# Performance work log

Measured on AMD Instinct MI355X. Metric: run time of the kernel, lower is better.

The kernel has to match this reference:

```python
import jax, jax.numpy as jnp
import numpy as np

B, T, D, H, L = 64, 4096, 128, 128, 2


def setup_inputs() -> dict:
    key = jax.random.key(0)
    ks = jax.random.split(key, 9)
    s = 1.0 / np.sqrt(H)
    return {
        "x": jax.random.normal(ks[0], (B, T, D), dtype=jnp.float32),
        "W_ih0": jax.random.normal(ks[1], (3 * H, D), dtype=jnp.float32) * s,
        "W_hh0": jax.random.normal(ks[2], (3 * H, H), dtype=jnp.float32) * s,
        "b_ih0": jax.random.normal(ks[3], (3 * H,), dtype=jnp.float32) * s,
        "b_hh0": jax.random.normal(ks[4], (3 * H,), dtype=jnp.float32) * s,
        "W_ih1": jax.random.normal(ks[5], (3 * H, H), dtype=jnp.float32) * s,
        "W_hh1": jax.random.normal(ks[6], (3 * H, H), dtype=jnp.float32) * s,
        "b_ih1": jax.random.normal(ks[7], (3 * H,), dtype=jnp.float32) * s,
        "b_hh1": jax.random.normal(ks[8], (3 * H,), dtype=jnp.float32) * s,
    }


def _gru_cell(h, xt, W_ih, W_hh, b_ih, b_hh):
    # torch.nn.GRUCell math; gates packed as [r, z, n] along 3H.
    gi = xt @ W_ih.T + b_ih            # [B, 3H]
    gh = h @ W_hh.T + b_hh             # [B, 3H]
    i_r, i_z, i_n = jnp.split(gi, 3, axis=-1)
    h_r, h_z, h_n = jnp.split(gh, 3, axis=-1)
    r = jax.nn.sigmoid(i_r + h_r)
    z = jax.nn.sigmoid(i_z + h_z)
    n = jnp.tanh(i_n + r * h_n)
    return (1.0 - z) * n + z * h


def reference(x, W_ih0, W_hh0, b_ih0, b_hh0, W_ih1, W_hh1, b_ih1, b_hh1):
    h0 = jnp.zeros((L, x.shape[0], H), dtype=x.dtype)
    params = ((W_ih0, W_hh0, b_ih0, b_hh0), (W_ih1, W_hh1, b_ih1, b_hh1))

    def step(h, xt):
        # h: [L, B, H]; xt: [B, D]
        inp = xt
        new_h = []
        for l in range(L):
            hl = _gru_cell(h[l], inp, *params[l])
            new_h.append(hl)
            inp = hl
        return jnp.stack(new_h, axis=0), None

    xs = jnp.swapaxes(x, 0, 1)  # [T, B, D]
    h_final, _ = jax.lax.scan(step, h0, xs)
    return h_final  # [L, B, H]
```

## Files before the change

kernel.cpp:

```cpp
#include <hip/hip_runtime.h>


#define Tlen 4096
#define Hd   128
#define Bsz  64

typedef __attribute__((ext_vector_type(8))) short short8;
typedef __attribute__((ext_vector_type(4))) short short4v;
typedef __attribute__((ext_vector_type(4))) float float4v;
typedef __attribute__((ext_vector_type(2))) unsigned int uint2v;

#define MFMA16(a, b, c) __builtin_amdgcn_mfma_f32_16x16x32_bf16((a), (b), (c), 0, 0, 0)

static __device__ __forceinline__ float fast_exp2(float x) {
#if __has_builtin(__builtin_amdgcn_exp2f)
  return __builtin_amdgcn_exp2f(x);
#else
  return exp2f(x);
#endif
}
static __device__ __forceinline__ float fast_rcp(float x) {
  return __builtin_amdgcn_rcpf(x);
}
static __device__ __forceinline__ short f2bf(float f) {
  unsigned u = __builtin_bit_cast(unsigned, f);
  u = (u + 0x7FFFu + ((u >> 16) & 1u)) >> 16;
  return (short)u;
}
static __device__ __forceinline__ unsigned pk2bf(float a, float b) {
#if __has_builtin(__builtin_amdgcn_cvt_pk_bf16_f32)
  auto v = __builtin_amdgcn_cvt_pk_bf16_f32(a, b);
  return __builtin_bit_cast(unsigned, v);
#else
  return (unsigned)(unsigned short)f2bf(a) | ((unsigned)(unsigned short)f2bf(b) << 16);
#endif
}
static __device__ __forceinline__ short8 loadw8(const float* __restrict__ p) {
  short8 r;
  #pragma unroll
  for (int j = 0; j < 8; ++j) r[j] = f2bf(p[j]);
  return r;
}

#define XB   0
#define H0B  4096
#define H1B  8192
#define BLK  2048

__global__ __launch_bounds__(512, 2) void gru_scan(
    const float* __restrict__ x,
    const float* __restrict__ Wih0, const float* __restrict__ Whh0,
    const float* __restrict__ bih0, const float* __restrict__ bhh0,
    const float* __restrict__ Wih1, const float* __restrict__ Whh1,
    const float* __restrict__ bih1, const float* __restrict__ bhh1,
    float* __restrict__ out) {
  __shared__ alignas(16) short Abuf[12288];

  const int tid   = threadIdx.x;
  const int wave  = tid >> 6;
  const int lane  = tid & 63;
  const int lc    = lane & 15;
  const int quad  = lane >> 4;
  const int q8    = quad * 8;
  const int lane8 = lane * 8;
  const int bbase = blockIdx.x * 16;

  const int wgrp = wave >> 2;
  const int w4   = wave & 3;

  const float* Wi = wgrp ? Wih1 : Wih0;
  const float* Wh = wgrp ? Whh1 : Whh0;
  const float* bi = wgrp ? bih1 : bih0;
  const float* bh = wgrp ? bhh1 : bhh0;

  short8 fxr[2][4], fxz[2][4], fxn[2][4];
  short8 fhr[2][4], fhz[2][4], fhn[2][4];
  float kr[2], kz[2], ki[2], kh[2];
  const float nL  = -1.44269504088896f;
  const float n2L = -2.88539008177793f;
  #pragma unroll
  for (int G = 0; G < 2; ++G) {
    const int c = 32 * w4 + 16 * G + lc;
    #pragma unroll
    for (int s = 0; s < 4; ++s) {
      const int k = 32 * s + q8;
      fxr[G][s] = loadw8(Wi + (c)       * Hd + k);
      fxz[G][s] = loadw8(Wi + (128 + c) * Hd + k);
      fxn[G][s] = loadw8(Wi + (256 + c) * Hd + k);
      fhr[G][s] = loadw8(Wh + (c)       * Hd + k);
      fhz[G][s] = loadw8(Wh + (128 + c) * Hd + k);
      fhn[G][s] = loadw8(Wh + (256 + c) * Hd + k);
    }
    kr[G] = nL  * (bi[c] + bh[c]);
    kz[G] = nL  * (bi[128 + c] + bh[128 + c]);
    ki[G] = n2L * bi[256 + c];
    kh[G] = n2L * bh[256 + c];
  }

  const int hsel = wgrp ? H1B : H0B;
  const int isel = wgrp ? H0B : XB;

  int hw[2];
  #pragma unroll
  for (int G = 0; G < 2; ++G)
    hw[G] = w4 * 512 + (2 * G + (lc >> 3)) * 128 + (lc & 7);

  const int xrow = tid >> 5;
  const int xk0  = 4 * (tid & 31);
  const int xwoff = (xk0 >> 5) * 512 + ((xk0 >> 3) & 3) * 128 + xrow * 8 + (xk0 & 7);
  const float* xg = x + (size_t)(bbase + xrow) * (Tlen * Hd) + xk0;

  const int glo = wgrp ? 2 : 0;
  const int ghi = glo + Tlen;

  {
    int* zb = (int*)Abuf;
    #pragma unroll
    for (int i = 0; i < 8; ++i) zb[2048 + tid + 512 * i] = 0;
    const float4v v0 = *(const float4v*)(xg);
    const float4v v1 = *(const float4v*)(xg + Hd);
    uint2v p0 = {pk2bf(v0[0], v0[1]), pk2bf(v0[2], v0[3])};
    uint2v p1 = {pk2bf(v1[0], v1[1]), pk2bf(v1[2], v1[3])};
    *(short4v*)&Abuf[XB + xwoff]       = __builtin_bit_cast(short4v, p0);
    *(short4v*)&Abuf[XB + BLK + xwoff] = __builtin_bit_cast(short4v, p1);
  }
  __syncthreads();

  const float4v Z4 = {0.f, 0.f, 0.f, 0.f};
  float4v ar[2], az[2], an[2], ah[2];
  float4v hp[2] = {Z4, Z4};

  #pragma unroll
  for (int G = 0; G < 2; ++G) { ar[G] = Z4; az[G] = Z4; an[G] = Z4; ah[G] = Z4; }
  #pragma unroll
  for (int s = 0; s < 4; ++s) {
    const short8 a = *(const short8*)&Abuf[isel + s * 512 + lane8];
    #pragma unroll
    for (int G = 0; G < 2; ++G) {
      ar[G] = MFMA16(a, fxr[G][s], ar[G]);
      az[G] = MFMA16(a, fxz[G][s], az[G]);
      an[G] = MFMA16(a, fxn[G][s], an[G]);
    }
  }

  for (int t = 0; t < Tlen + 2; ++t) {
    const int par  = (t & 1) * BLK;
    const int parx = BLK - par;

    const int tn = (t + 2 < Tlen) ? (t + 2) : (Tlen - 1);
    const float4v xv = *(const float4v*)(xg + (size_t)tn * Hd);
    const int hrd = hsel + parx;
    #pragma unroll
    for (int s = 0; s < 4; ++s) {
      const short8 a = *(const short8*)&Abuf[hrd + s * 512 + lane8];
      #pragma unroll
      for (int G = 0; G < 2; ++G) {
        ar[G] = MFMA16(a, fhr[G][s], ar[G]);
        az[G] = MFMA16(a, fhz[G][s], az[G]);
        ah[G] = MFMA16(a, fhn[G][s], ah[G]);
      }
    }
    __syncthreads();

    if (t >= glo && t < ghi) {
      const int wr = hsel + par;
      #pragma unroll
      for (int G = 0; G < 2; ++G) {
        #pragma unroll
        for (int i = 0; i < 4; ++i) {
          const float er = fast_exp2(fmaf(ar[G][i], nL, kr[G]));
          const float rr = fast_rcp(1.0f + er);
          const float ez = fast_exp2(fmaf(az[G][i], nL, kz[G]));
          const float zz = fast_rcp(1.0f + ez);
          float vv = fmaf(rr, fmaf(ah[G][i], n2L, kh[G]),
                          fmaf(an[G][i], n2L, ki[G]));
          vv = fminf(vv, 126.0f);
          const float e2 = fast_exp2(vv);
          const float nn = (1.0f - e2) * fast_rcp(1.0f + e2);
          const float hn = fmaf(zz, hp[G][i] - nn, nn);
          hp[G][i] = hn;
          Abuf[wr + hw[G] + (quad * 4 + i) * 8] = f2bf(hn);
        }
      }
    }
    {
      uint2v pp = {pk2bf(xv[0], xv[1]), pk2bf(xv[2], xv[3])};
      *(short4v*)&Abuf[XB + par + xwoff] = __builtin_bit_cast(short4v, pp);
    }
    const int ird = isel + parx;
    #pragma unroll
    for (int G = 0; G < 2; ++G) { ar[G] = Z4; az[G] = Z4; an[G] = Z4; ah[G] = Z4; }
    #pragma unroll
    for (int s = 0; s < 4; ++s) {
      const short8 a = *(const short8*)&Abuf[ird + s * 512 + lane8];
      #pragma unroll
      for (int G = 0; G < 2; ++G) {
        ar[G] = MFMA16(a, fxr[G][s], ar[G]);
        az[G] = MFMA16(a, fxz[G][s], az[G]);
        an[G] = MFMA16(a, fxn[G][s], an[G]);
      }
    }
    __syncthreads();
  }

  #pragma unroll
  for (int G = 0; G < 2; ++G) {
    const int u = 32 * w4 + 16 * G + lc;
    #pragma unroll
    for (int i = 0; i < 4; ++i) {
      const int b = bbase + quad * 4 + i;
      out[wgrp * (Bsz * Hd) + b * Hd + u] = hp[G][i];
    }
  }
}

extern "C" void kernel_launch(void* const* d_in, const int* in_sizes, int n_in,
                              void* d_out, int out_size, void* d_ws, size_t ws_size,
                              hipStream_t stream) {
  (void)in_sizes; (void)n_in; (void)out_size; (void)d_ws; (void)ws_size;
  gru_scan<<<4, 512, 0, stream>>>(
      (const float*)d_in[0],
      (const float*)d_in[1], (const float*)d_in[2],
      (const float*)d_in[3], (const float*)d_in[4],
      (const float*)d_in[5], (const float*)d_in[6],
      (const float*)d_in[7], (const float*)d_in[8],
      (float*)d_out);
}
```

Measured before the change: 7.178 ms.

## Merge per-step input and hidden GEMMs into one phase with a single barrier

The time loop is restructured so each step loads both input and hidden operands, does all MFMAs, then the gate math, with one __syncthreads per step instead of two. Layer 1 now runs one step behind layer 0 instead of two. The MFMA operands are swapped so weights are the A operand, which transposes the output layout. This lets each lane write four consecutive hidden units with one packed bf16 store instead of four scalar stores. The cost is a longer serial chain between barriers, with input and hidden MFMAs no longer overlapped across the barrier, plus a partial unroll by 2.

Result: slower. 15.48 ms (+115.7%).

```diff
diff --git a/kernel.cpp b/kernel.cpp
--- a/kernel.cpp
+++ b/kernel.cpp
@@ -73,143 +73,138 @@
   const float* bi = wgrp ? bih1 : bih0;
   const float* bh = wgrp ? bhh1 : bhh0;
 
-  short8 fxr[2][4], fxz[2][4], fxn[2][4];
-  short8 fhr[2][4], fhz[2][4], fhn[2][4];
-  float kr[2], kz[2], ki[2], kh[2];
+  short8 wxr[2][4], wxz[2][4], wxn[2][4];
+  short8 whr[2][4], whz[2][4], whn[2][4];
+  float kr[2][4], kz[2][4], ki[2][4], kh[2][4];
   const float nL  = -1.44269504088896f;
   const float n2L = -2.88539008177793f;
   #pragma unroll
-  for (int G = 0; G < 2; ++G) {
-    const int c = 32 * w4 + 16 * G + lc;
+  for (int T = 0; T < 2; ++T) {
+    const int U0 = 32 * w4 + 16 * T;
     #pragma unroll
     for (int s = 0; s < 4; ++s) {
       const int k = 32 * s + q8;
-      fxr[G][s] = loadw8(Wi + (c)       * Hd + k);
-      fxz[G][s] = loadw8(Wi + (128 + c) * Hd + k);
-      fxn[G][s] = loadw8(Wi + (256 + c) * Hd + k);
-      fhr[G][s] = loadw8(Wh + (c)       * Hd + k);
-      fhz[G][s] = loadw8(Wh + (128 + c) * Hd + k);
-      fhn[G][s] = loadw8(Wh + (256 + c) * Hd + k);
-    }
-    kr[G] = nL  * (bi[c] + bh[c]);
-    kz[G] = nL  * (bi[128 + c] + bh[128 + c]);
-    ki[G] = n2L * bi[256 + c];
-    kh[G] = n2L * bh[256 + c];
-  }
-
-  const int hsel = wgrp ? H1B : H0B;
-  const int isel = wgrp ? H0B : XB;
-
-  int hw[2];
-  #pragma unroll
-  for (int G = 0; G < 2; ++G)
-    hw[G] = w4 * 512 + (2 * G + (lc >> 3)) * 128 + (lc & 7);
-
-  const int xrow = tid >> 5;
-  const int xk0  = 4 * (tid & 31);
+      wxr[T][s] = loadw8(Wi + (U0 + lc) * Hd + k);
+      wxz[T][s] = loadw8(Wi + (128 + U0 + lc) * Hd + k);
+      wxn[T][s] = loadw8(Wi + (256 + U0 + lc) * Hd + k);
+      whr[T][s] = loadw8(Wh + (U0 + lc) * Hd + k);
+      whz[T][s] = loadw8(Wh + (128 + U0 + lc) * Hd + k);
+      whn[T][s] = loadw8(Wh + (256 + U0 + lc) * Hd + k);
+    }
+    #pragma unroll
+    for (int i = 0; i < 4; ++i) {
+      const int U = U0 + quad * 4 + i;
+      kr[T][i] = nL  * (bi[U] + bh[U]);
+      kz[T][i] = nL  * (bi[128 + U] + bh[128 + U]);
+      ki[T][i] = n2L * bi[256 + U];
+      kh[T][i] = n2L * bh[256 + U];
+    }
+  }
+
+  const int ib0 = wgrp ? H0B : XB;
+  const int hb0 = wgrp ? H1B : H0B;
+
+  int wroff[2];
+  #pragma unroll
+  for (int T = 0; T < 2; ++T)
+    wroff[T] = w4 * 512 + (2 * T + (quad >> 1)) * 128 + lc * 8 + 4 * (quad & 1);
+
+  const int xrow  = tid >> 5;
+  const int xk0   = 4 * (tid & 31);
   const int xwoff = (xk0 >> 5) * 512 + ((xk0 >> 3) & 3) * 128 + xrow * 8 + (xk0 & 7);
   const float* xg = x + (size_t)(bbase + xrow) * (Tlen * Hd) + xk0;
 
-  const int glo = wgrp ? 2 : 0;
-  const int ghi = glo + Tlen;
-
   {
     int* zb = (int*)Abuf;
     #pragma unroll
     for (int i = 0; i < 8; ++i) zb[2048 + tid + 512 * i] = 0;
     const float4v v0 = *(const float4v*)(xg);
-    const float4v v1 = *(const float4v*)(xg + Hd);
-    uint2v p0 = {pk2bf(v0[0], v0[1]), pk2bf(v0[2], v0[3])};
-    uint2v p1 = {pk2bf(v1[0], v1[1]), pk2bf(v1[2], v1[3])};
-    *(short4v*)&Abuf[XB + xwoff]       = __builtin_bit_cast(short4v, p0);
-    *(short4v*)&Abuf[XB + BLK + xwoff] = __builtin_bit_cast(short4v, p1);
+    uint2v pp = {pk2bf(v0[0], v0[1]), pk2bf(v0[2], v0[3])};
+    *(short4v*)&Abuf[XB + xwoff] = __builtin_bit_cast(short4v, pp);
   }
   __syncthreads();
 
   const float4v Z4 = {0.f, 0.f, 0.f, 0.f};
-  float4v ar[2], az[2], an[2], ah[2];
   float4v hp[2] = {Z4, Z4};
 
-  #pragma unroll
-  for (int G = 0; G < 2; ++G) { ar[G] = Z4; az[G] = Z4; an[G] = Z4; ah[G] = Z4; }
-  #pragma unroll
-  for (int s = 0; s < 4; ++s) {
-    const short8 a = *(const short8*)&Abuf[isel + s * 512 + lane8];
-    #pragma unroll
-    for (int G = 0; G < 2; ++G) {
-      ar[G] = MFMA16(a, fxr[G][s], ar[G]);
-      az[G] = MFMA16(a, fxz[G][s], az[G]);
-      an[G] = MFMA16(a, fxn[G][s], an[G]);
-    }
-  }
-
-  for (int t = 0; t < Tlen + 2; ++t) {
-    const int par  = (t & 1) * BLK;
-    const int parx = BLK - par;
-
-    const int tn = (t + 2 < Tlen) ? (t + 2) : (Tlen - 1);
+  #pragma unroll 2
+  for (int t = 0; t <= Tlen; ++t) {
+    const int ibase = ib0 + ((t + wgrp) & 1) * BLK;
+    const int hbase = hb0 + ((t + 1 + wgrp) & 1) * BLK;
+    const int wbase = hb0 + ((t + wgrp) & 1) * BLK;
+
+    const int tn = (t + 1 < Tlen) ? (t + 1) : (Tlen - 1);
     const float4v xv = *(const float4v*)(xg + (size_t)tn * Hd);
-    const int hrd = hsel + parx;
-    #pragma unroll
-    for (int s = 0; s < 4; ++s) {
-      const short8 a = *(const short8*)&Abuf[hrd + s * 512 + lane8];
+
+    short8 bfi[4], bfh[4];
+    #pragma unroll
+    for (int s = 0; s < 4; ++s)
+      bfi[s] = *(const short8*)&Abuf[ibase + s * 512 + lane8];
+    #pragma unroll
+    for (int s = 0; s < 4; ++s)
+      bfh[s] = *(const short8*)&Abuf[hbase + s * 512 + lane8];
+
+    float4v aR[2], aZ[2], aIN[2], aHN[2];
+    #pragma unroll
+    for (int T = 0; T < 2; ++T) {
+      aR[T]  = MFMA16(wxr[T][0], bfi[0], Z4);
+      aZ[T]  = MFMA16(wxz[T][0], bfi[0], Z4);
+      aIN[T] = MFMA16(wxn[T][0], bfi[0], Z4);
+      aHN[T] = MFMA16(whn[T][0], bfh[0], Z4);
       #pragma unroll
-      for (int G = 0; G < 2; ++G) {
-        ar[G] = MFMA16(a, fhr[G][s], ar[G]);
-        az[G] = MFMA16(a, fhz[G][s], az[G]);
-        ah[G] = MFMA16(a, fhn[G][s], ah[G]);
-      }
-    }
-    __syncthreads();
-
-    if (t >= glo && t < ghi) {
-      const int wr = hsel + par;
+      for (int s = 1; s < 4; ++s) {
+        aR[T]  = MFMA16(wxr[T][s], bfi[s], aR[T]);
+        aZ[T]  = MFMA16(wxz[T][s], bfi[s], aZ[T]);
+        aIN[T] = MFMA16(wxn[T][s], bfi[s], aIN[T]);
+        aHN[T] = MFMA16(whn[T][s], bfh[s], aHN[T]);
+      }
       #pragma unroll
-      for (int G = 0; G < 2; ++G) {
+      for (int s = 0; s < 4; ++s) {
+        aR[T] = MFMA16(whr[T][s], bfh[s], aR[T]);
+        aZ[T] = MFMA16(whz[T][s], bfh[s], aZ[T]);
+      }
+    }
+
+    const bool gv = wgrp ? (t >= 1) : (t < Tlen);
+    #pragma unroll
+    for (int T = 0; T < 2; ++T) {
+      float hn[4];
+      #pragma unroll
+      for (int i = 0; i < 4; ++i) {
+        const float er = fast_exp2(fmaf(aR[T][i], nL, kr[T][i]));
+        const float rr = fast_rcp(1.0f + er);
+        const float ez = fast_exp2(fmaf(aZ[T][i], nL, kz[T][i]));
+        const float zz = fast_rcp(1.0f + ez);
+        float vv = fmaf(rr, fmaf(aHN[T][i], n2L, kh[T][i]),
+                        fmaf(aIN[T][i], n2L, ki[T][i]));
+        vv = fminf(vv, 126.0f);
+        const float e2 = fast_exp2(vv);
+        const float nn = (1.0f - e2) * fast_rcp(1.0f + e2);
+        hn[i] = fmaf(zz, hp[T][i] - nn, nn);
+      }
+      if (gv) {
         #pragma unroll
-        for (int i = 0; i < 4; ++i) {
-          const float er = fast_exp2(fmaf(ar[G][i], nL, kr[G]));
-          const float rr = fast_rcp(1.0f + er);
-          const float ez = fast_exp2(fmaf(az[G][i], nL, kz[G]));
-          const float zz = fast_rcp(1.0f + ez);
-          float vv = fmaf(rr, fmaf(ah[G][i], n2L, kh[G]),
-                          fmaf(an[G][i], n2L, ki[G]));
-          vv = fminf(vv, 126.0f);
-          const float e2 = fast_exp2(vv);
-          const float nn = (1.0f - e2) * fast_rcp(1.0f + e2);
-          const float hn = fmaf(zz, hp[G][i] - nn, nn);
-          hp[G][i] = hn;
-          Abuf[wr + hw[G] + (quad * 4 + i) * 8] = f2bf(hn);
-        }
-      }
-    }
+        for (int i = 0; i < 4; ++i) hp[T][i] = hn[i];
+        uint2v pp = {pk2bf(hn[0], hn[1]), pk2bf(hn[2], hn[3])};
+        *(short4v*)&Abuf[wbase + wroff[T]] = __builtin_bit_cast(short4v, pp);
+      }
+    }
+
     {
       uint2v pp = {pk2bf(xv[0], xv[1]), pk2bf(xv[2], xv[3])};
-      *(short4v*)&Abuf[XB + par + xwoff] = __builtin_bit_cast(short4v, pp);
-    }
-    const int ird = isel + parx;
-    #pragma unroll
-    for (int G = 0; G < 2; ++G) { ar[G] = Z4; az[G] = Z4; an[G] = Z4; ah[G] = Z4; }
-    #pragma unroll
-    for (int s = 0; s < 4; ++s) {
-      const short8 a = *(const short8*)&Abuf[ird + s * 512 + lane8];
-      #pragma unroll
-      for (int G = 0; G < 2; ++G) {
-        ar[G] = MFMA16(a, fxr[G][s], ar[G]);
-        az[G] = MFMA16(a, fxz[G][s], az[G]);
-        an[G] = MFMA16(a, fxn[G][s], an[G]);
-      }
+      *(short4v*)&Abuf[XB + ((t + 1) & 1) * BLK + xwoff] =
+          __builtin_bit_cast(short4v, pp);
     }
     __syncthreads();
   }
 
   #pragma unroll
-  for (int G = 0; G < 2; ++G) {
-    const int u = 32 * w4 + 16 * G + lc;
+  for (int T = 0; T < 2; ++T) {
     #pragma unroll
     for (int i = 0; i < 4; ++i) {
-      const int b = bbase + quad * 4 + i;
-      out[wgrp * (Bsz * Hd) + b * Hd + u] = hp[G][i];
+      const int u = 32 * w4 + 16 * T + quad * 4 + i;
+      const int b = bbase + lc;
+      out[wgrp * (Bsz * Hd) + b * Hd + u] = hp[T][i];
     }
   }
 }
```

## Precompute layer-0 input projection in a parallel pre-kernel and restructure scan

Applied to the files above, without the earlier changes.

Adds a separate highly parallel kernel that computes x@W_ih0 for all timesteps into workspace as bf16, taking that GEMM off the sequential recurrence. The scan kernel now has all 8 waves handle both layers for a 16-unit slice each, with layer-1 hidden-dependent work overlapped with layer 0. It prefetches the precomputed gates two steps ahead and falls back to the old kernel when workspace is too small. This adds global traffic for the gate buffer and extra bf16 rounding of the input gates.

Measured after the change: 7.391 ms. +3.0%, slower.

```diff
diff --git a/kernel.cpp b/kernel.cpp
--- a/kernel.cpp
+++ b/kernel.cpp
@@ -9,6 +9,7 @@
 typedef __attribute__((ext_vector_type(4))) short short4v;
 typedef __attribute__((ext_vector_type(4))) float float4v;
 typedef __attribute__((ext_vector_type(2))) unsigned int uint2v;
+typedef __attribute__((ext_vector_type(4))) unsigned int uint4v;
 
 #define MFMA16(a, b, c) __builtin_amdgcn_mfma_f32_16x16x32_bf16((a), (b), (c), 0, 0, 0)
 
@@ -41,13 +42,252 @@
   for (int j = 0; j < 8; ++j) r[j] = f2bf(p[j]);
   return r;
 }
-
-#define XB   0
-#define H0B  4096
-#define H1B  8192
+static __device__ __forceinline__ float bfsel(uint2v d, int i) {
+  const unsigned u = (i & 1) ? (d[i >> 1] & 0xFFFF0000u) : (d[i >> 1] << 16);
+  return __builtin_bit_cast(float, u);
+}
+
+__global__ __launch_bounds__(512, 2) void gru_pre(
+    const float* __restrict__ x, const float* __restrict__ Wih0,
+    short* __restrict__ G) {
+  const int tid  = threadIdx.x;
+  const int w    = tid >> 6;
+  const int lane = tid & 63;
+  const int lc   = lane & 15;
+  const int quad = lane >> 4;
+  const int q8   = quad * 8;
+  const int bb   = blockIdx.x & 3;
+  const int c    = blockIdx.x >> 2;
+
+  short8 fr[4], fz[4], fn[4];
+  #pragma unroll
+  for (int s = 0; s < 4; ++s) {
+    const int k = 32 * s + q8;
+    fr[s] = loadw8(Wih0 + (16 * w + lc) * Hd + k);
+    fz[s] = loadw8(Wih0 + (128 + 16 * w + lc) * Hd + k);
+    fn[s] = loadw8(Wih0 + (256 + 16 * w + lc) * Hd + k);
+  }
+  const float* xrow = x + (size_t)(bb * 16 + lc) * (Tlen * Hd);
+  const float4v Z4 = {0.f, 0.f, 0.f, 0.f};
+
+  for (int tt = 0; tt < 128; ++tt) {
+    const int t = c * 128 + tt;
+    short8 bx[4];
+    #pragma unroll
+    for (int s = 0; s < 4; ++s) {
+      const float* p = xrow + (size_t)t * Hd + 32 * s + q8;
+      const float4v lo = *(const float4v*)p;
+      const float4v hi = *(const float4v*)(p + 4);
+      uint4v u = {pk2bf(lo[0], lo[1]), pk2bf(lo[2], lo[3]),
+                  pk2bf(hi[0], hi[1]), pk2bf(hi[2], hi[3])};
+      bx[s] = __builtin_bit_cast(short8, u);
+    }
+    float4v gr = Z4, gz = Z4, gn = Z4;
+    #pragma unroll
+    for (int s = 0; s < 4; ++s) {
+      gr = MFMA16(fr[s], bx[s], gr);
+      gz = MFMA16(fz[s], bx[s], gz);
+      gn = MFMA16(fn[s], bx[s], gn);
+    }
+    const size_t base = ((((size_t)bb * Tlen + t) * 8 + w) * 3) * 256;
+    uint2v pr = {pk2bf(gr[0], gr[1]), pk2bf(gr[2], gr[3])};
+    uint2v pz = {pk2bf(gz[0], gz[1]), pk2bf(gz[2], gz[3])};
+    uint2v pn = {pk2bf(gn[0], gn[1]), pk2bf(gn[2], gn[3])};
+    *(uint2v*)&G[base + 0 * 256 + lane * 4] = pr;
+    *(uint2v*)&G[base + 1 * 256 + lane * 4] = pz;
+    *(uint2v*)&G[base + 2 * 256 + lane * 4] = pn;
+  }
+}
+
+#define CH0  0
+#define CH1  4096
 #define BLK  2048
 
 __global__ __launch_bounds__(512, 2) void gru_scan(
+    const float* __restrict__ Whh0,
+    const float* __restrict__ bih0, const float* __restrict__ bhh0,
+    const float* __restrict__ Wih1, const float* __restrict__ Whh1,
+    const float* __restrict__ bih1, const float* __restrict__ bhh1,
+    const short* __restrict__ G, float* __restrict__ out) {
+  __shared__ alignas(16) short Abuf[8192];
+
+  const int tid   = threadIdx.x;
+  const int w     = tid >> 6;
+  const int lane  = tid & 63;
+  const int lc    = lane & 15;
+  const int quad  = lane >> 4;
+  const int q8    = quad * 8;
+  const int lane8 = lane * 8;
+  const int bbase = blockIdx.x * 16;
+
+  short8 whr0[4], whz0[4], whn0[4];
+  short8 wxr1[4], wxz1[4], wxn1[4];
+  short8 whr1[4], whz1[4], whn1[4];
+  #pragma unroll
+  for (int s = 0; s < 4; ++s) {
+    const int k = 32 * s + q8;
+    const int ur = 16 * w + lc, uz = 128 + 16 * w + lc, un = 256 + 16 * w + lc;
+    whr0[s] = loadw8(Whh0 + ur * Hd + k);
+    whz0[s] = loadw8(Whh0 + uz * Hd + k);
+    whn0[s] = loadw8(Whh0 + un * Hd + k);
+    wxr1[s] = loadw8(Wih1 + ur * Hd + k);
+    wxz1[s] = loadw8(Wih1 + uz * Hd + k);
+    wxn1[s] = loadw8(Wih1 + un * Hd + k);
+    whr1[s] = loadw8(Whh1 + ur * Hd + k);
+    whz1[s] = loadw8(Whh1 + uz * Hd + k);
+    whn1[s] = loadw8(Whh1 + un * Hd + k);
+  }
+
+  const float nL  = -1.44269504088896f;
+  const float n2L = -2.88539008177793f;
+  float kr0[4], kz0[4], ki0[4], kh0[4], kr1[4], kz1[4], ki1[4], kh1[4];
+  #pragma unroll
+  for (int i = 0; i < 4; ++i) {
+    const int u = 16 * w + quad * 4 + i;
+    kr0[i] = nL  * (bih0[u] + bhh0[u]);
+    kz0[i] = nL  * (bih0[128 + u] + bhh0[128 + u]);
+    ki0[i] = n2L * bih0[256 + u];
+    kh0[i] = n2L * bhh0[256 + u];
+    kr1[i] = nL  * (bih1[u] + bhh1[u]);
+    kz1[i] = nL  * (bih1[128 + u] + bhh1[128 + u]);
+    ki1[i] = n2L * bih1[256 + u];
+    kh1[i] = n2L * bhh1[256 + u];
+  }
+
+  const int wroff = (w >> 1) * 512 + ((2 * w + (quad >> 1)) & 3) * 128 +
+                    lc * 8 + 4 * (quad & 1);
+
+  const char* Gp = (const char*)G;
+  const size_t gbase = (((size_t)blockIdx.x * Tlen * 8 + w) * 3) * 512 + lane * 8;
+
+  {
+    int* zb = (int*)Abuf;
+    #pragma unroll
+    for (int i = 0; i < 8; ++i) zb[tid + 512 * i] = 0;
+  }
+  uint2v G2[2][3];
+  #pragma unroll
+  for (int g = 0; g < 3; ++g) {
+    G2[0][g] = *(const uint2v*)(Gp + gbase + g * 512);
+    G2[1][g] = *(const uint2v*)(Gp + gbase + 12288 + g * 512);
+  }
+  __syncthreads();
+
+  const float4v Z4 = {0.f, 0.f, 0.f, 0.f};
+  float4v aR = Z4, aZ = Z4, aHN = Z4;
+  float4v cR = Z4, cZ = Z4, cIN = Z4, cHN = Z4;
+  float h0p[4] = {0.f, 0.f, 0.f, 0.f};
+  float h1p[4] = {0.f, 0.f, 0.f, 0.f};
+
+  #pragma unroll 2
+  for (int t = 0; t < Tlen + 2; ++t) {
+    const int p = t & 1;
+
+    short8 hf[4];
+    #pragma unroll
+    for (int s = 0; s < 4; ++s)
+      hf[s] = *(const short8*)&Abuf[CH0 + (p ^ 1) * BLK + s * 512 + lane8];
+
+    if (t >= 2) {
+      float hn[4];
+      #pragma unroll
+      for (int i = 0; i < 4; ++i) {
+        const float er = fast_exp2(fmaf(cR[i], nL, kr1[i]));
+        const float rr = fast_rcp(1.0f + er);
+        const float ez = fast_exp2(fmaf(cZ[i], nL, kz1[i]));
+        const float zz = fast_rcp(1.0f + ez);
+        float vv = fmaf(rr, fmaf(cHN[i], n2L, kh1[i]),
+                        fmaf(cIN[i], n2L, ki1[i]));
+        vv = fminf(vv, 126.0f);
+        const float e2 = fast_exp2(vv);
+        const float nn = (1.0f - e2) * fast_rcp(1.0f + e2);
+        hn[i] = fmaf(zz, h1p[i] - nn, nn);
+        h1p[i] = hn[i];
+      }
+      uint2v pp = {pk2bf(hn[0], hn[1]), pk2bf(hn[2], hn[3])};
+      *(short4v*)&Abuf[CH1 + p * BLK + wroff] = __builtin_bit_cast(short4v, pp);
+    }
+
+    aR  = MFMA16(whr0[0], hf[0], Z4);
+    aZ  = MFMA16(whz0[0], hf[0], Z4);
+    aHN = MFMA16(whn0[0], hf[0], Z4);
+    cR  = MFMA16(wxr1[0], hf[0], Z4);
+    cZ  = MFMA16(wxz1[0], hf[0], Z4);
+    cIN = MFMA16(wxn1[0], hf[0], Z4);
+    #pragma unroll
+    for (int s = 1; s < 4; ++s) {
+      aR  = MFMA16(whr0[s], hf[s], aR);
+      aZ  = MFMA16(whz0[s], hf[s], aZ);
+      aHN = MFMA16(whn0[s], hf[s], aHN);
+      cR  = MFMA16(wxr1[s], hf[s], cR);
+      cZ  = MFMA16(wxz1[s], hf[s], cZ);
+      cIN = MFMA16(wxn1[s], hf[s], cIN);
+    }
+    __syncthreads();
+
+    short8 gf[4];
+    #pragma unroll
+    for (int s = 0; s < 4; ++s)
+      gf[s] = *(const short8*)&Abuf[CH1 + p * BLK + s * 512 + lane8];
+
+    if (t < Tlen) {
+      float hn[4];
+      #pragma unroll
+      for (int i = 0; i < 4; ++i) {
+        const float gr = bfsel(G2[p][0], i);
+        const float gz = bfsel(G2[p][1], i);
+        const float gn = bfsel(G2[p][2], i);
+        const float er = fast_exp2(fmaf(aR[i] + gr, nL, kr0[i]));
+        const float rr = fast_rcp(1.0f + er);
+        const float ez = fast_exp2(fmaf(aZ[i] + gz, nL, kz0[i]));
+        const float zz = fast_rcp(1.0f + ez);
+        float vv = fmaf(rr, fmaf(aHN[i], n2L, kh0[i]),
+                        fmaf(gn, n2L, ki0[i]));
+        vv = fminf(vv, 126.0f);
+        const float e2 = fast_exp2(vv);
+        const float nn = (1.0f - e2) * fast_rcp(1.0f + e2);
+        hn[i] = fmaf(zz, h0p[i] - nn, nn);
+        h0p[i] = hn[i];
+      }
+      uint2v pp = {pk2bf(hn[0], hn[1]), pk2bf(hn[2], hn[3])};
+      *(short4v*)&Abuf[CH0 + p * BLK + wroff] = __builtin_bit_cast(short4v, pp);
+    }
+
+    cHN = MFMA16(whn1[0], gf[0], Z4);
+    cR  = MFMA16(whr1[0], gf[0], cR);
+    cZ  = MFMA16(whz1[0], gf[0], cZ);
+    #pragma unroll
+    for (int s = 1; s < 4; ++s) {
+      cHN = MFMA16(whn1[s], gf[s], cHN);
+      cR  = MFMA16(whr1[s], gf[s], cR);
+      cZ  = MFMA16(whz1[s], gf[s], cZ);
+    }
+
+    {
+      const int tg = (t + 2 < Tlen) ? (t + 2) : (Tlen - 1);
+      const size_t go = gbase + (size_t)tg * 12288;
+      #pragma unroll
+      for (int g = 0; g < 3; ++g)
+        G2[p][g] = *(const uint2v*)(Gp + go + g * 512);
+    }
+    __syncthreads();
+  }
+
+  #pragma unroll
+  for (int i = 0; i < 4; ++i) {
+    const int u = 16 * w + quad * 4 + i;
+    const int b = bbase + lc;
+    out[b * Hd + u]            = h0p[i];
+    out[Bsz * Hd + b * Hd + u] = h1p[i];
+  }
+}
+
+#define FXB   0
+#define FH0B  4096
+#define FH1B  8192
+#define FBLK  2048
+
+__global__ __launch_bounds__(512, 2) void gru_scan_fb(
     const float* __restrict__ x,
     const float* __restrict__ Wih0, const float* __restrict__ Whh0,
     const float* __restrict__ bih0, const float* __restrict__ bhh0,
@@ -64,7 +304,6 @@
   const int q8    = quad * 8;
   const int lane8 = lane * 8;
   const int bbase = blockIdx.x * 16;
-
   const int wgrp = wave >> 2;
   const int w4   = wave & 3;
 
@@ -79,40 +318,35 @@
   const float nL  = -1.44269504088896f;
   const float n2L = -2.88539008177793f;
   #pragma unroll
-  for (int G = 0; G < 2; ++G) {
-    const int c = 32 * w4 + 16 * G + lc;
+  for (int Gg = 0; Gg < 2; ++Gg) {
+    const int c = 32 * w4 + 16 * Gg + lc;
     #pragma unroll
     for (int s = 0; s < 4; ++s) {
       const int k = 32 * s + q8;
-      fxr[G][s] = loadw8(Wi + (c)       * Hd + k);
-      fxz[G][s] = loadw8(Wi + (128 + c) * Hd + k);
-      fxn[G][s] = loadw8(Wi + (256 + c) * Hd + k);
-      fhr[G][s] = loadw8(Wh + (c)       * Hd + k);
-      fhz[G][s] = loadw8(Wh + (128 + c) * Hd + k);
-      fhn[G][s] = loadw8(Wh + (256 + c) * Hd + k);
-    }
-    kr[G] = nL  * (bi[c] + bh[c]);
-    kz[G] = nL  * (bi[128 + c] + bh[128 + c]);
-    ki[G] = n2L * bi[256 + c];
-    kh[G] = n2L * bh[256 + c];
-  }
-
-  const int hsel = wgrp ? H1B : H0B;
-  const int isel = wgrp ? H0B : XB;
-
+      fxr[Gg][s] = loadw8(Wi + (c) * Hd + k);
+      fxz[Gg][s] = loadw8(Wi + (128 + c) * Hd + k);
+      fxn[Gg][s] = loadw8(Wi + (256 + c) * Hd + k);
+      fhr[Gg][s] = loadw8(Wh + (c) * Hd + k);
+      fhz[Gg][s] = loadw8(Wh + (128 + c) * Hd + k);
+      fhn[Gg][s] = loadw8(Wh + (256 + c) * Hd + k);
+    }
+    kr[Gg] = nL  * (bi[c] + bh[c]);
+    kz[Gg] = nL  * (bi[128 + c] + bh[128 + c]);
+    ki[Gg] = n2L * bi[256 + c];
+    kh[Gg] = n2L * bh[256 + c];
+  }
+  const int hsel = wgrp ? FH1B : FH0B;
+  const int isel = wgrp ? FH0B : FXB;
   int hw[2];
   #pragma unroll
-  for (int G = 0; G < 2; ++G)
-    hw[G] = w4 * 512 + (2 * G + (lc >> 3)) * 128 + (lc & 7);
-
+  for (int Gg = 0; Gg < 2; ++Gg)
+    hw[Gg] = w4 * 512 + (2 * Gg + (lc >> 3)) * 128 + (lc & 7);
   const int xrow = tid >> 5;
   const int xk0  = 4 * (tid & 31);
   const int xwoff = (xk0 >> 5) * 512 + ((xk0 >> 3) & 3) * 128 + xrow * 8 + (xk0 & 7);
   const float* xg = x + (size_t)(bbase + xrow) * (Tlen * Hd) + xk0;
-
   const int glo = wgrp ? 2 : 0;
   const int ghi = glo + Tlen;
-
   {
     int* zb = (int*)Abuf;
     #pragma unroll
@@ -121,32 +355,28 @@
     const float4v v1 = *(const float4v*)(xg + Hd);
     uint2v p0 = {pk2bf(v0[0], v0[1]), pk2bf(v0[2], v0[3])};
     uint2v p1 = {pk2bf(v1[0], v1[1]), pk2bf(v1[2], v1[3])};
-    *(short4v*)&Abuf[XB + xwoff]       = __builtin_bit_cast(short4v, p0);
-    *(short4v*)&Abuf[XB + BLK + xwoff] = __builtin_bit_cast(short4v, p1);
+    *(short4v*)&Abuf[FXB + xwoff]        = __builtin_bit_cast(short4v, p0);
+    *(short4v*)&Abuf[FXB + FBLK + xwoff] = __builtin_bit_cast(short4v, p1);
   }
   __syncthreads();
-
   const float4v Z4 = {0.f, 0.f, 0.f, 0.f};
   float4v ar[2], az[2], an[2], ah[2];
   float4v hp[2] = {Z4, Z4};
-
-  #pragma unroll
-  for (int G = 0; G < 2; ++G) { ar[G] = Z4; az[G] = Z4; an[G] = Z4; ah[G] = Z4; }
+  #pragma unroll
+  for (int Gg = 0; Gg < 2; ++Gg) { ar[Gg] = Z4; az[Gg] = Z4; an[Gg] = Z4; ah[Gg] = Z4; }
   #pragma unroll
   for (int s = 0; s < 4; ++s) {
     const short8 a = *(const short8*)&Abuf[isel + s * 512 + lane8];
     #pragma unroll
-    for (int G = 0; G < 2; ++G) {
-      ar[G] = MFMA16(a, fxr[G][s], ar[G]);
-      az[G] = MFMA16(a, fxz[G][s], az[G]);
-      an[G] = MFMA16(a, fxn[G][s], an[G]);
-    }
-  }
-
+    for (int Gg = 0; Gg < 2; ++Gg) {
+      ar[Gg] = MFMA16(a, fxr[Gg][s], ar[Gg]);
+      az[Gg] = MFMA16(a, fxz[Gg][s], az[Gg]);
+      an[Gg] = MFMA16(a, fxn[Gg][s], an[Gg]);
+    }
+  }
   for (int t = 0; t < Tlen + 2; ++t) {
-    const int par  = (t & 1) * BLK;
-    const int parx = BLK - par;
-
+    const int par  = (t & 1) * FBLK;
+    const int parx = FBLK - par;
     const int tn = (t + 2 < Tlen) ? (t + 2) : (Tlen - 1);
     const float4v xv = *(const float4v*)(xg + (size_t)tn * Hd);
     const int hrd = hsel + parx;
@@ -154,62 +384,60 @@
     for (int s = 0; s < 4; ++s) {
       const short8 a = *(const short8*)&Abuf[hrd + s * 512 + lane8];
       #pragma unroll
-      for (int G = 0; G < 2; ++G) {
-        ar[G] = MFMA16(a, fhr[G][s], ar[G]);
-        az[G] = MFMA16(a, fhz[G][s], az[G]);
-        ah[G] = MFMA16(a, fhn[G][s], ah[G]);
+      for (int Gg = 0; Gg < 2; ++Gg) {
+        ar[Gg] = MFMA16(a, fhr[Gg][s], ar[Gg]);
+        az[Gg] = MFMA16(a, fhz[Gg][s], az[Gg]);
+        ah[Gg] = MFMA16(a, fhn[Gg][s], ah[Gg]);
       }
     }
     __syncthreads();
-
     if (t >= glo && t < ghi) {
       const int wr = hsel + par;
       #pragma unroll
-      for (int G = 0; G < 2; ++G) {
+      for (int Gg = 0; Gg < 2; ++Gg) {
         #pragma unroll
         for (int i = 0; i < 4; ++i) {
-          const float er = fast_exp2(fmaf(ar[G][i], nL, kr[G]));
+          const float er = fast_exp2(fmaf(ar[Gg][i], nL, kr[Gg]));
           const float rr = fast_rcp(1.0f + er);
-          const float ez = fast_exp2(fmaf(az[G][i], nL, kz[G]));
+          const float ez = fast_exp2(fmaf(az[Gg][i], nL, kz[Gg]));
           const float zz = fast_rcp(1.0f + ez);
-          float vv = fmaf(rr, fmaf(ah[G][i], n2L, kh[G]),
-                          fmaf(an[G][i], n2L, ki[G]));
+          float vv = fmaf(rr, fmaf(ah[Gg][i], n2L, kh[Gg]),
+                          fmaf(an[Gg][i], n2L, ki[Gg]));
           vv = fminf(vv, 126.0f);
           const float e2 = fast_exp2(vv);
           const float nn = (1.0f - e2) * fast_rcp(1.0f + e2);
-          const float hn = fmaf(zz, hp[G][i] - nn, nn);
-          hp[G][i] = hn;
-          Abuf[wr + hw[G] + (quad * 4 + i) * 8] = f2bf(hn);
+          const float hn = fmaf(zz, hp[Gg][i] - nn, nn);
+          hp[Gg][i] = hn;
+          Abuf[wr + hw[Gg] + (quad * 4 + i) * 8] = f2bf(hn);
         }
       }
     }
     {
       uint2v pp = {pk2bf(xv[0], xv[1]), pk2bf(xv[2], xv[3])};
-      *(short4v*)&Abuf[XB + par + xwoff] = __builtin_bit_cast(short4v, pp);
+      *(short4v*)&Abuf[FXB + par + xwoff] = __builtin_bit_cast(short4v, pp);
     }
     const int ird = isel + parx;
     #pragma unroll
-    for (int G = 0; G < 2; ++G) { ar[G] = Z4; az[G] = Z4; an[G] = Z4; ah[G] = Z4; }
+    for (int Gg = 0; Gg < 2; ++Gg) { ar[Gg] = Z4; az[Gg] = Z4; an[Gg] = Z4; ah[Gg] = Z4; }
     #pragma unroll
     for (int s = 0; s < 4; ++s) {
       const short8 a = *(const short8*)&Abuf[ird + s * 512 + lane8];
       #pragma unroll
-      for (int G = 0; G < 2; ++G) {
-        ar[G] = MFMA16(a, fxr[G][s], ar[G]);
-        az[G] = MFMA16(a, fxz[G][s], az[G]);
-        an[G] = MFMA16(a, fxn[G][s], an[G]);
+      for (int Gg = 0; Gg < 2; ++Gg) {
+        ar[Gg] = MFMA16(a, fxr[Gg][s], ar[Gg]);
+        az[Gg] = MFMA16(a, fxz[Gg][s], az[Gg]);
+        an[Gg] = MFMA16(a, fxn[Gg][s], an[Gg]);
       }
     }
     __syncthreads();
   }
-
-  #pragma unroll
-  for (int G = 0; G < 2; ++G) {
-    const int u = 32 * w4 + 16 * G + lc;
+  #pragma unroll
+  for (int Gg = 0; Gg < 2; ++Gg) {
+    const int u = 32 * w4 + 16 * Gg + lc;
     #pragma unroll
     for (int i = 0; i < 4; ++i) {
       const int b = bbase + quad * 4 + i;
-      out[wgrp * (Bsz * Hd) + b * Hd + u] = hp[G][i];
+      out[wgrp * (Bsz * Hd) + b * Hd + u] = hp[Gg][i];
     }
   }
 }
@@ -217,12 +445,24 @@
 extern "C" void kernel_launch(void* const* d_in, const int* in_sizes, int n_in,
                               void* d_out, int out_size, void* d_ws, size_t ws_size,
                               hipStream_t stream) {
-  (void)in_sizes; (void)n_in; (void)out_size; (void)d_ws; (void)ws_size;
-  gru_scan<<<4, 512, 0, stream>>>(
-      (const float*)d_in[0],
-      (const float*)d_in[1], (const float*)d_in[2],
-      (const float*)d_in[3], (const float*)d_in[4],
-      (const float*)d_in[5], (const float*)d_in[6],
-      (const float*)d_in[7], (const float*)d_in[8],
-      (float*)d_out);
-}
+  (void)in_sizes; (void)n_in; (void)out_size;
+  const size_t G_bytes = (size_t)4 * Tlen * 8 * 3 * 64 * 4 * 2;
+  if (ws_size >= G_bytes) {
+    gru_pre<<<128, 512, 0, stream>>>(
+        (const float*)d_in[0], (const float*)d_in[1], (short*)d_ws);
+    gru_scan<<<4, 512, 0, stream>>>(
+        (const float*)d_in[2],
+        (const float*)d_in[3], (const float*)d_in[4],
+        (const float*)d_in[5], (const float*)d_in[6],
+        (const float*)d_in[7], (const float*)d_in[8],
+        (const short*)d_ws, (float*)d_out);
+  } else {
+    gru_scan_fb<<<4, 512, 0, stream>>>(
+        (const float*)d_in[0],
+        (const float*)d_in[1], (const float*)d_in[2],
+        (const float*)d_in[3], (const float*)d_in[4],
+        (const float*)d_in[5], (const float*)d_in[6],
+        (const float*)d_in[7], (const float*)d_in[8],
+        (float*)d_out);
+  }
+}
```
